# Performance work log

Measured on AMD Instinct MI355X. Metric: run time of the kernel, lower is better.

Reference implementation:

```python
import jax, jax.numpy as jnp
import numpy as np

B, S, E, H = 4, 2048, 512, 8
DH = E // H
EPS = 1e-5

def _ln(x, g, b):
    m = jnp.mean(x, axis=-1, keepdims=True)
    v = jnp.var(x, axis=-1, keepdims=True)
    return (x - m) * jax.lax.rsqrt(v + EPS) * g + b

def setup_inputs() -> dict:
    key = jax.random.key(0)
    ks = jax.random.split(key, 8)
    sc = 0.02
    return {
        "x": jax.random.normal(ks[0], (B, S, E), dtype=jnp.float32),
        "ln1_g": jnp.ones((E,), jnp.float32),
        "ln1_b": jnp.zeros((E,), jnp.float32),
        "in_proj_w": sc * jax.random.normal(ks[1], (3 * E, E), jnp.float32),
        "in_proj_b": jnp.zeros((3 * E,), jnp.float32),
        "out_w": sc * jax.random.normal(ks[2], (E, E), jnp.float32),
        "out_b": jnp.zeros((E,), jnp.float32),
        "ln2_g": jnp.ones((E,), jnp.float32),
        "ln2_b": jnp.zeros((E,), jnp.float32),
        "fc1_w": sc * jax.random.normal(ks[3], (E, E), jnp.float32),
        "fc1_b": jnp.zeros((E,), jnp.float32),
        "fc2_w": sc * jax.random.normal(ks[4], (E, E), jnp.float32),
        "fc2_b": jnp.zeros((E,), jnp.float32),
    }

def reference(x, ln1_g, ln1_b, in_proj_w, in_proj_b, out_w, out_b,
              ln2_g, ln2_b, fc1_w, fc1_b, fc2_w, fc2_b):
    # pre-LN
    z = _ln(x, ln1_g, ln1_b)
    # qkv projection (torch MHA packed in_proj: [3E, E])
    qkv = z @ in_proj_w.T + in_proj_b          # [B,S,3E]
    q, k, v = jnp.split(qkv, 3, axis=-1)
    q = q.reshape(B, S, H, DH)
    k = k.reshape(B, S, H, DH)
    v = v.reshape(B, S, H, DH)
    scores = jnp.einsum("bqhd,bkhd->bhqk", q, k) / np.sqrt(DH).astype(np.float32)
    causal = jnp.triu(jnp.ones((S, S), dtype=bool), k=1)  # True = masked
    neg = jnp.finfo(scores.dtype).min
    scores = jnp.where(causal, neg, scores)
    attn = jax.nn.softmax(scores, axis=-1)      # [B,H,S,S]
    ctx = jnp.einsum("bhqk,bkhd->bqhd", attn, v).reshape(B, S, E)
    attn_out = ctx @ out_w.T + out_b
    # torch MHA with need_weights=True averages over heads by default
    attn_weights = jnp.mean(attn, axis=1)       # [B,S,S]
    z2 = x + attn_out
    y = _ln(z2, ln2_g, ln2_b)
    y = jax.nn.leaky_relu(y @ fc1_w.T + fc1_b, negative_slope=0.01)
    y = y @ fc2_w.T + fc2_b
    y = y + z2
    return (y, attn_weights)
```

## Files before the change

### kernel.cpp

```cpp
#include <hip/hip_runtime.h>

typedef short bf16x8 __attribute__((ext_vector_type(8)));
typedef float f32x4 __attribute__((ext_vector_type(4)));
typedef unsigned short u16x8 __attribute__((ext_vector_type(8)));

#define NB 4
#define SQ 2048
#define EM 512
#define NH 8
#define DHD 64
#define QSCALE 0.1803368801111731f

__device__ __forceinline__ unsigned short f2bf(float x) {
  unsigned u = __float_as_uint(x);
  u += 0x7FFFu + ((u >> 16) & 1u);
  return (unsigned short)(u >> 16);
}

__device__ __forceinline__ int sw8(int row, int col8) { return col8 ^ ((row & 7) << 3); }

__device__ __forceinline__ void glds16(const void* g, void* l) {
  __builtin_amdgcn_global_load_lds(
      (const __attribute__((address_space(1))) void*)g,
      (__attribute__((address_space(3))) void*)l, 16, 0, 0);
}

__global__ __launch_bounds__(256) void f2bf4_kernel(
    const float* __restrict__ w0, const float* __restrict__ w1,
    const float* __restrict__ w2, const float* __restrict__ w3,
    unsigned short* __restrict__ o0, unsigned short* __restrict__ o1,
    unsigned short* __restrict__ o2, unsigned short* __restrict__ o3) {
  int i = (blockIdx.x * 256 + threadIdx.x) * 8;
  const float* src;
  unsigned short* dst;
  int off;
  if (i < 786432) { src = w0; dst = o0; off = i; }
  else if (i < 1048576) { src = w1; dst = o1; off = i - 786432; }
  else if (i < 1310720) { src = w2; dst = o2; off = i - 1048576; }
  else { src = w3; dst = o3; off = i - 1310720; }
  f32x4 a = *(const f32x4*)(src + off);
  f32x4 b = *(const f32x4*)(src + off + 4);
  u16x8 o;
#pragma unroll
  for (int j = 0; j < 4; ++j) { o[j] = f2bf(a[j]); o[j + 4] = f2bf(b[j]); }
  *(u16x8*)(dst + off) = o;
}

__global__ __launch_bounds__(256) void ln_kernel(const float* __restrict__ x,
                                                 const float* __restrict__ g,
                                                 const float* __restrict__ bb,
                                                 unsigned short* __restrict__ out) {
  int tid = threadIdx.x;
  int row = blockIdx.x * 4 + (tid >> 6);
  int lane = tid & 63;
  size_t base = (size_t)row * EM + lane * 8;
  f32x4 v0 = *(const f32x4*)(x + base);
  f32x4 v1 = *(const f32x4*)(x + base + 4);
  float s = 0.f, q = 0.f;
#pragma unroll
  for (int j = 0; j < 4; ++j) { s += v0[j] + v1[j]; q += v0[j] * v0[j] + v1[j] * v1[j]; }
#pragma unroll
  for (int m = 1; m < 64; m <<= 1) { s += __shfl_xor(s, m); q += __shfl_xor(q, m); }
  float mean = s * (1.f / EM);
  float var = q * (1.f / EM) - mean * mean;
  float rs = rsqrtf(var + 1e-5f);
  f32x4 g0 = *(const f32x4*)(g + lane * 8), g1 = *(const f32x4*)(g + lane * 8 + 4);
  f32x4 b0 = *(const f32x4*)(bb + lane * 8), b1 = *(const f32x4*)(bb + lane * 8 + 4);
  u16x8 o;
#pragma unroll
  for (int j = 0; j < 4; ++j) {
    o[j] = f2bf((v0[j] - mean) * rs * g0[j] + b0[j]);
    o[j + 4] = f2bf((v1[j] - mean) * rs * g1[j] + b1[j]);
  }
  *(u16x8*)(out + base) = o;
}

template <bool LEAKY, bool RESID, bool OUTF32, bool QKV>
__global__ __launch_bounds__(256) void gemm64(
    const unsigned short* __restrict__ A, const unsigned short* __restrict__ Bm,
    const float* __restrict__ bias, const float* __restrict__ resid,
    float* __restrict__ outf, unsigned short* __restrict__ outh,
    unsigned short* __restrict__ qo, unsigned short* __restrict__ ko,
    unsigned short* __restrict__ vo, int M, int N, int K) {
  __shared__ unsigned short As[2][64][64];
  __shared__ unsigned short Bs[2][64][64];
  int m0 = blockIdx.x * 64, n0 = blockIdx.y * 64;
  int t = threadIdx.x;
  int wv = t >> 6, ln = t & 63, lg = ln >> 4, lr = ln & 15;
  int rsub = ln >> 3;
  int csw = ((ln & 7) ^ rsub) * 8;
  f32x4 acc[4];
#pragma unroll
  for (int c = 0; c < 4; ++c)
#pragma unroll
    for (int r = 0; r < 4; ++r) acc[c][r] = 0.f;

  const unsigned short* ag0 = A + (size_t)(m0 + wv * 16 + rsub) * K + csw;
  const unsigned short* ag1 = A + (size_t)(m0 + wv * 16 + 8 + rsub) * K + csw;
  const unsigned short* bg0 = Bm + (size_t)(n0 + wv * 16 + rsub) * K + csw;
  const unsigned short* bg1 = Bm + (size_t)(n0 + wv * 16 + 8 + rsub) * K + csw;

  glds16(ag0, &As[0][wv * 16][0]);
  glds16(ag1, &As[0][wv * 16 + 8][0]);
  glds16(bg0, &Bs[0][wv * 16][0]);
  glds16(bg1, &Bs[0][wv * 16 + 8][0]);

  int nk = K >> 6;
  for (int ki = 0; ki < nk; ++ki) {
    int cur = ki & 1;
    __syncthreads();
    if (ki + 1 < nk) {
      int nb = cur ^ 1;
      int ko_ = (ki + 1) * 64;
      glds16(ag0 + ko_, &As[nb][wv * 16][0]);
      glds16(ag1 + ko_, &As[nb][wv * 16 + 8][0]);
      glds16(bg0 + ko_, &Bs[nb][wv * 16][0]);
      glds16(bg1 + ko_, &Bs[nb][wv * 16 + 8][0]);
    }
#pragma unroll
    for (int kk = 0; kk < 64; kk += 32) {
      int arw = wv * 16 + lr;
      bf16x8 af = *(const bf16x8*)&As[cur][arw][sw8(arw, kk + lg * 8)];
#pragma unroll
      for (int c = 0; c < 4; ++c) {
        int brw = c * 16 + lr;
        bf16x8 bf = *(const bf16x8*)&Bs[cur][brw][sw8(brw, kk + lg * 8)];
        acc[c] = __builtin_amdgcn_mfma_f32_16x16x32_bf16(af, bf, acc[c], 0, 0, 0);
      }
    }
  }
#pragma unroll
  for (int c = 0; c < 4; ++c) {
    int C_ = n0 + c * 16 + lr;
    float bv = bias[C_];
#pragma unroll
    for (int r = 0; r < 4; ++r) {
      int R_ = m0 + wv * 16 + lg * 4 + r;
      float v = acc[c][r] + bv;
      if (LEAKY) v = v > 0.f ? v : 0.01f * v;
      if (RESID) v += resid[(size_t)R_ * N + C_];
      if (QKV) {
        int which = C_ >> 9, f = C_ & 511, h = f >> 6, d = f & 63;
        int b_ = R_ >> 11, s_ = R_ & 2047;
        if (which == 0) {
          qo[(((size_t)b_ * NH + h) * SQ + s_) * DHD + d] = f2bf(v * QSCALE);
        } else if (which == 1) {
          ko[(((size_t)b_ * NH + h) * SQ + s_) * DHD + d] = f2bf(v);
        } else {
          vo[(((size_t)b_ * NH + h) * DHD + d) * SQ + s_] = f2bf(v);
        }
      } else if (OUTF32) {
        outf[(size_t)R_ * N + C_] = v;
      } else {
        outh[(size_t)R_ * N + C_] = f2bf(v);
      }
    }
  }
}

__global__ __launch_bounds__(256) void gemm128qkv(
    const unsigned short* __restrict__ A, const unsigned short* __restrict__ Bm,
    const float* __restrict__ bias, unsigned short* __restrict__ qo,
    unsigned short* __restrict__ ko, unsigned short* __restrict__ vo, int K) {
  __shared__ unsigned short As[2][128][32];
  __shared__ unsigned short Bs[2][128][32];
  int lin = blockIdx.x;
  int xcd = lin & 7, idx = lin >> 3;
  int m0 = (xcd * 8 + (idx & 7)) * 128;
  int n0 = (idx >> 3) * 128;
  int t = threadIdx.x;
  int wv = t >> 6, ln = t & 63, lg = ln >> 4, lr = ln & 15;
  int wr = wv >> 1, wc = wv & 1;
  int row16 = ln >> 2, chunk = (ln & 3) * 8;
  f32x4 acc[4][4];
#pragma unroll
  for (int m = 0; m < 4; ++m)
#pragma unroll
    for (int n = 0; n < 4; ++n)
#pragma unroll
      for (int r = 0; r < 4; ++r) acc[m][n][r] = 0.f;

  const unsigned short* agA = A + (size_t)(m0 + wv * 16 + row16) * K + chunk;
  const unsigned short* agB = A + (size_t)(m0 + 64 + wv * 16 + row16) * K + chunk;
  const unsigned short* bgA = Bm + (size_t)(n0 + wv * 16 + row16) * K + chunk;
  const unsigned short* bgB = Bm + (size_t)(n0 + 64 + wv * 16 + row16) * K + chunk;

  glds16(agA, &As[0][wv * 16][0]);
  glds16(agB, &As[0][64 + wv * 16][0]);
  glds16(bgA, &Bs[0][wv * 16][0]);
  glds16(bgB, &Bs[0][64 + wv * 16][0]);

  int nk = K >> 5;
  for (int ki = 0; ki < nk; ++ki) {
    int cur = ki & 1;
    __syncthreads();
    if (ki + 1 < nk) {
      int nb = cur ^ 1;
      int ko_ = (ki + 1) * 32;
      glds16(agA + ko_, &As[nb][wv * 16][0]);
      glds16(agB + ko_, &As[nb][64 + wv * 16][0]);
      glds16(bgA + ko_, &Bs[nb][wv * 16][0]);
      glds16(bgB + ko_, &Bs[nb][64 + wv * 16][0]);
    }
    bf16x8 af[4], bfr[4];
#pragma unroll
    for (int m = 0; m < 4; ++m)
      af[m] = *(const bf16x8*)&As[cur][wr * 64 + m * 16 + lr][lg * 8];
#pragma unroll
    for (int n = 0; n < 4; ++n)
      bfr[n] = *(const bf16x8*)&Bs[cur][wc * 64 + n * 16 + lr][lg * 8];
#pragma unroll
    for (int m = 0; m < 4; ++m)
#pragma unroll
      for (int n = 0; n < 4; ++n)
        acc[m][n] = __builtin_amdgcn_mfma_f32_16x16x32_bf16(af[m], bfr[n], acc[m][n], 0, 0, 0);
  }

#pragma unroll
  for (int n = 0; n < 4; ++n) {
    int C_ = n0 + wc * 64 + n * 16 + lr;
    float bv = bias[C_];
#pragma unroll
    for (int m = 0; m < 4; ++m) {
#pragma unroll
      for (int r = 0; r < 4; ++r) {
        int R_ = m0 + wr * 64 + m * 16 + lg * 4 + r;
        float v = acc[m][n][r] + bv;
        int which = C_ >> 9, f = C_ & 511, h = f >> 6, d = f & 63;
        int b_ = R_ >> 11, s_ = R_ & 2047;
        if (which == 0) {
          qo[(((size_t)b_ * NH + h) * SQ + s_) * DHD + d] = f2bf(v * QSCALE);
        } else if (which == 1) {
          ko[(((size_t)b_ * NH + h) * SQ + s_) * DHD + d] = f2bf(v);
        } else {
          vo[(((size_t)b_ * NH + h) * DHD + d) * SQ + s_] = f2bf(v);
        }
      }
    }
  }
}

__global__ __launch_bounds__(256) void flash_kernel(
    const unsigned short* __restrict__ Q, const unsigned short* __restrict__ Kb,
    const unsigned short* __restrict__ Vt, unsigned short* __restrict__ ctx,
    float* __restrict__ mstat, float* __restrict__ lstat) {
  __shared__ unsigned short Ks[2][64][64];
  __shared__ unsigned short Vs[2][64][64];
  __shared__ unsigned short Ps[4][16][64];
  int lin = blockIdx.x;
  int xcd = lin & 7, idx = lin >> 3;
  int qt = 31 - (idx >> 2);
  int grp = xcd + 8 * (idx & 3);
  int h = grp & 7, b = grp >> 3;
  int qb = qt * 64;
  int t = threadIdx.x, wv = t >> 6, ln = t & 63, lg = ln >> 4, lr = ln & 15;
  int rsub = ln >> 3;
  int csw = ((ln & 7) ^ rsub) * 8;
  size_t headoff = ((size_t)b * NH + h) * SQ;
  const unsigned short* kg0 = Kb + (headoff + wv * 16 + rsub) * DHD + csw;
  const unsigned short* kg1 = Kb + (headoff + wv * 16 + 8 + rsub) * DHD + csw;
  const unsigned short* vg0 = Vt + (((size_t)b * NH + h) * DHD + wv * 16 + rsub) * SQ + csw;
  const unsigned short* vg1 = Vt + (((size_t)b * NH + h) * DHD + wv * 16 + 8 + rsub) * SQ + csw;

  const unsigned short* qrow = Q + (headoff + qb + wv * 16 + lr) * DHD;
  bf16x8 aq0 = *(const bf16x8*)(qrow + lg * 8);
  bf16x8 aq1 = *(const bf16x8*)(qrow + 32 + lg * 8);

  bf16x8 vones;
#pragma unroll
  for (int j = 0; j < 8; ++j) vones[j] = (lr == 0) ? (short)0x3F80 : (short)0;

  f32x4 cacc[4], lacc;
#pragma unroll
  for (int nd = 0; nd < 4; ++nd)
#pragma unroll
    for (int r = 0; r < 4; ++r) cacc[nd][r] = 0.f;
#pragma unroll
  for (int r = 0; r < 4; ++r) lacc[r] = 0.f;
  float mrun[4];
#pragma unroll
  for (int r = 0; r < 4; ++r) mrun[r] = -__builtin_inff();

  int nkt = qt + 1;
  glds16(kg0, &Ks[0][wv * 16][0]);
  glds16(kg1, &Ks[0][wv * 16 + 8][0]);
  glds16(vg0, &Vs[0][wv * 16][0]);
  glds16(vg1, &Vs[0][wv * 16 + 8][0]);

  for (int kt = 0; kt < nkt; ++kt) {
    int cur = kt & 1;
    __syncthreads();
    if (kt + 1 < nkt) {
      int nb = cur ^ 1;
      size_t ko_ = (size_t)(kt + 1) * 64;
      glds16(kg0 + ko_ * DHD, &Ks[nb][wv * 16][0]);
      glds16(kg1 + ko_ * DHD, &Ks[nb][wv * 16 + 8][0]);
      glds16(vg0 + ko_, &Vs[nb][wv * 16][0]);
      glds16(vg1 + ko_, &Vs[nb][wv * 16 + 8][0]);
    }

    float sv[4][4];
    __builtin_amdgcn_s_setprio(1);
#pragma unroll
    for (int nt = 0; nt < 4; ++nt) {
      f32x4 sf;
#pragma unroll
      for (int r = 0; r < 4; ++r) sf[r] = 0.f;
      int brw = nt * 16 + lr;
      bf16x8 bk0 = *(const bf16x8*)&Ks[cur][brw][sw8(brw, lg * 8)];
      bf16x8 bk1 = *(const bf16x8*)&Ks[cur][brw][sw8(brw, 32 + lg * 8)];
      sf = __builtin_amdgcn_mfma_f32_16x16x32_bf16(aq0, bk0, sf, 0, 0, 0);
      sf = __builtin_amdgcn_mfma_f32_16x16x32_bf16(aq1, bk1, sf, 0, 0, 0);
#pragma unroll
      for (int r = 0; r < 4; ++r) sv[nt][r] = sf[r];
    }
    __builtin_amdgcn_s_setprio(0);
    if (kt == nkt - 1) {
      int kbase = kt * 64;
#pragma unroll
      for (int nt = 0; nt < 4; ++nt) {
        int kcol = kbase + nt * 16 + lr;
#pragma unroll
        for (int r = 0; r < 4; ++r) {
          int qr = qb + wv * 16 + lg * 4 + r;
          if (kcol > qr) sv[nt][r] = -__builtin_inff();
        }
      }
    }

    float lmax[4];
    bool need = false;
#pragma unroll
    for (int r = 0; r < 4; ++r) {
      lmax[r] = fmaxf(fmaxf(sv[0][r], sv[1][r]), fmaxf(sv[2][r], sv[3][r]));
      need |= (lmax[r] > mrun[r] + 8.f);
    }
    if (__any(need)) {
#pragma unroll
      for (int r = 0; r < 4; ++r) {
        float tm = lmax[r];
#pragma unroll
        for (int m = 1; m < 16; m <<= 1) tm = fmaxf(tm, __shfl_xor(tm, m));
        float mn = fmaxf(mrun[r], tm);
        float sc = exp2f(mrun[r] - mn);
        mrun[r] = mn;
        lacc[r] *= sc;
#pragma unroll
        for (int nd = 0; nd < 4; ++nd) cacc[nd][r] *= sc;
      }
    }
#pragma unroll
    for (int r = 0; r < 4; ++r) {
      int prow = lg * 4 + r;
#pragma unroll
      for (int nt = 0; nt < 4; ++nt) {
        float p = exp2f(sv[nt][r] - mrun[r]);
        Ps[wv][prow][sw8(prow, nt * 16 + lr)] =
            (unsigned short)(__float_as_uint(p) >> 16);
      }
    }

    bf16x8 pf0 = *(const bf16x8*)&Ps[wv][lr][sw8(lr, lg * 8)];
    bf16x8 pf1 = *(const bf16x8*)&Ps[wv][lr][sw8(lr, 32 + lg * 8)];
    __builtin_amdgcn_s_setprio(1);
    lacc = __builtin_amdgcn_mfma_f32_16x16x32_bf16(pf0, vones, lacc, 0, 0, 0);
    lacc = __builtin_amdgcn_mfma_f32_16x16x32_bf16(pf1, vones, lacc, 0, 0, 0);
#pragma unroll
    for (int nd = 0; nd < 4; ++nd) {
      int vrw = nd * 16 + lr;
      bf16x8 vf0 = *(const bf16x8*)&Vs[cur][vrw][sw8(vrw, lg * 8)];
      bf16x8 vf1 = *(const bf16x8*)&Vs[cur][vrw][sw8(vrw, 32 + lg * 8)];
      cacc[nd] = __builtin_amdgcn_mfma_f32_16x16x32_bf16(pf0, vf0, cacc[nd], 0, 0, 0);
      cacc[nd] = __builtin_amdgcn_mfma_f32_16x16x32_bf16(pf1, vf1, cacc[nd], 0, 0, 0);
    }
    __builtin_amdgcn_s_setprio(0);
  }

  float inv[4];
#pragma unroll
  for (int r = 0; r < 4; ++r) inv[r] = 1.f / __shfl(lacc[r], ln & 48);
#pragma unroll
  for (int nd = 0; nd < 4; ++nd)
#pragma unroll
    for (int r = 0; r < 4; ++r) {
      size_t dst = ((size_t)b * SQ + qb + wv * 16 + lg * 4 + r) * EM + h * DHD + nd * 16 + lr;
      ctx[dst] = f2bf(cacc[nd][r] * inv[r]);
    }
  if (lr == 0) {
#pragma unroll
    for (int r = 0; r < 4; ++r) {
      int row = qb + wv * 16 + lg * 4 + r;
      mstat[headoff + row] = mrun[r];
      lstat[headoff + row] = 0.125f * inv[r];
    }
  }
}

__global__ __launch_bounds__(256) void attnw_kernel(
    const unsigned short* __restrict__ Q, const unsigned short* __restrict__ Kb,
    const float* __restrict__ mstat, const float* __restrict__ lstat,
    float* __restrict__ aw) {
  int lin = blockIdx.x;
  int xcd = lin & 7, slot = lin >> 3;
  int combo = xcd + 8 * (slot >> 5);
  int qt = slot & 31;
  int kt2 = combo & 15, b = combo >> 4;
  int qb = qt * 64, kb = kt2 * 128;
  int t = threadIdx.x;
  float* tile = aw + ((size_t)b * SQ + qb) * SQ + kb;
  if (2 * kt2 > qt) {
    int row = t >> 2, cbase = (t & 3) * 32;
    f32x4 z;
#pragma unroll
    for (int j = 0; j < 4; ++j) z[j] = 0.f;
    float* p = tile + (size_t)row * SQ + cbase;
#pragma unroll
    for (int j = 0; j < 8; ++j) *(f32x4*)(p + j * 4) = z;
    return;
  }
  __shared__ unsigned short Ks[2][2][64][64];
  int wv = t >> 6, ln = t & 63, lg = ln >> 4, lr = ln & 15;
  int rsub = ln >> 3;
  int csw = ((ln & 7) ^ rsub) * 8;
  size_t khstride = (size_t)SQ * DHD;
  const unsigned short* kg00 = Kb + (((size_t)b * NH) * SQ + kb + wv * 16 + rsub) * DHD + csw;
  const unsigned short* kg01 = kg00 + (size_t)8 * DHD;
  const unsigned short* kg10 = kg00 + (size_t)64 * DHD;
  const unsigned short* kg11 = kg00 + (size_t)72 * DHD;
  const unsigned short* qg = Q + (((size_t)b * NH) * SQ + qb + wv * 16 + lr) * DHD + lg * 8;
  size_t mbase = (size_t)b * NH * SQ + qb + wv * 16 + lg * 4;

  glds16(kg00, &Ks[0][0][wv * 16][0]);
  glds16(kg01, &Ks[0][0][wv * 16 + 8][0]);
  glds16(kg10, &Ks[0][1][wv * 16][0]);
  glds16(kg11, &Ks[0][1][wv * 16 + 8][0]);

  bf16x8 aqc0 = *(const bf16x8*)qg;
  bf16x8 aqc1 = *(const bf16x8*)(qg + 32);
  bf16x8 aqn0 = *(const bf16x8*)(qg + khstride);
  bf16x8 aqn1 = *(const bf16x8*)(qg + khstride + 32);
  float mmc[4], lic[4], mmn[4], lin_[4];
#pragma unroll
  for (int r = 0; r < 4; ++r) {
    mmc[r] = mstat[mbase + r];
    lic[r] = lstat[mbase + r];
    mmn[r] = mstat[mbase + SQ + r];
    lin_[r] = lstat[mbase + SQ + r];
  }

  f32x4 facc[2][4];
#pragma unroll
  for (int j = 0; j < 2; ++j)
#pragma unroll
    for (int nt = 0; nt < 4; ++nt)
#pragma unroll
      for (int r = 0; r < 4; ++r) facc[j][nt][r] = 0.f;

  for (int h = 0; h < NH; ++h) {
    int cur = h & 1;
    __syncthreads();
    if (h + 1 < NH) {
      size_t ho = (size_t)(h + 1) * khstride;
      glds16(kg00 + ho, &Ks[cur ^ 1][0][wv * 16][0]);
      glds16(kg01 + ho, &Ks[cur ^ 1][0][wv * 16 + 8][0]);
      glds16(kg10 + ho, &Ks[cur ^ 1][1][wv * 16][0]);
      glds16(kg11 + ho, &Ks[cur ^ 1][1][wv * 16 + 8][0]);
    }

#pragma unroll
    for (int nt = 0; nt < 4; ++nt) {
      int brw = nt * 16 + lr;
      f32x4 sf0, sf1;
#pragma unroll
      for (int r = 0; r < 4; ++r) { sf0[r] = 0.f; sf1[r] = 0.f; }
      bf16x8 bk00 = *(const bf16x8*)&Ks[cur][0][brw][sw8(brw, lg * 8)];
      bf16x8 bk01 = *(const bf16x8*)&Ks[cur][0][brw][sw8(brw, 32 + lg * 8)];
      bf16x8 bk10 = *(const bf16x8*)&Ks[cur][1][brw][sw8(brw, lg * 8)];
      bf16x8 bk11 = *(const bf16x8*)&Ks[cur][1][brw][sw8(brw, 32 + lg * 8)];
      sf0 = __builtin_amdgcn_mfma_f32_16x16x32_bf16(aqc0, bk00, sf0, 0, 0, 0);
      sf1 = __builtin_amdgcn_mfma_f32_16x16x32_bf16(aqc0, bk10, sf1, 0, 0, 0);
      sf0 = __builtin_amdgcn_mfma_f32_16x16x32_bf16(aqc1, bk01, sf0, 0, 0, 0);
      sf1 = __builtin_amdgcn_mfma_f32_16x16x32_bf16(aqc1, bk11, sf1, 0, 0, 0);
#pragma unroll
      for (int r = 0; r < 4; ++r) {
        facc[0][nt][r] += exp2f(sf0[r] - mmc[r]) * lic[r];
        facc[1][nt][r] += exp2f(sf1[r] - mmc[r]) * lic[r];
      }
    }

    aqc0 = aqn0; aqc1 = aqn1;
#pragma unroll
    for (int r = 0; r < 4; ++r) { mmc[r] = mmn[r]; lic[r] = lin_[r]; }
    if (h + 2 < NH) {
      aqn0 = *(const bf16x8*)(qg + (size_t)(h + 2) * khstride);
      aqn1 = *(const bf16x8*)(qg + (size_t)(h + 2) * khstride + 32);
#pragma unroll
      for (int r = 0; r < 4; ++r) {
        mmn[r] = mstat[mbase + (size_t)(h + 2) * SQ + r];
        lin_[r] = lstat[mbase + (size_t)(h + 2) * SQ + r];
      }
    }
  }

#pragma unroll
  for (int j = 0; j < 2; ++j) {
    int ktj = 2 * kt2 + j;
    bool fullmask = (ktj > qt);
    bool dg = (ktj == qt);
#pragma unroll
    for (int nt = 0; nt < 4; ++nt) {
      int kc = kb + j * 64 + nt * 16 + lr;
#pragma unroll
      for (int r = 0; r < 4; ++r) {
        int qr = qb + wv * 16 + lg * 4 + r;
        float v = (fullmask || (dg && kc > qr)) ? 0.f : facc[j][nt][r];
        tile[(size_t)(wv * 16 + lg * 4 + r) * SQ + j * 64 + nt * 16 + lr] = v;
      }
    }
  }
}

extern "C" void kernel_launch(void* const* d_in, const int* in_sizes, int n_in,
                              void* d_out, int out_size, void* d_ws, size_t ws_size,
                              hipStream_t stream) {
  (void)in_sizes; (void)n_in; (void)out_size; (void)ws_size;
  const float* x = (const float*)d_in[0];
  const float* ln1g = (const float*)d_in[1];
  const float* ln1b = (const float*)d_in[2];
  const float* wqkv = (const float*)d_in[3];
  const float* bqkv = (const float*)d_in[4];
  const float* wout = (const float*)d_in[5];
  const float* bout = (const float*)d_in[6];
  const float* ln2g = (const float*)d_in[7];
  const float* ln2b = (const float*)d_in[8];
  const float* wfc1 = (const float*)d_in[9];
  const float* bfc1 = (const float*)d_in[10];
  const float* wfc2 = (const float*)d_in[11];
  const float* bfc2 = (const float*)d_in[12];

  char* ws = (char*)d_ws;
  unsigned short* zctx = (unsigned short*)(ws);
  unsigned short* qb_ = (unsigned short*)(ws + 8388608);
  unsigned short* kb_ = (unsigned short*)(ws + 16777216);
  unsigned short* vb_ = (unsigned short*)(ws + 25165824);
  float* z2 = (float*)(ws + 33554432);
  float* mstat = (float*)(ws + 50331648);
  float* lstat = (float*)(ws + 50593792);
  unsigned short* wqkv_h = (unsigned short*)(ws + 50855936);
  unsigned short* wout_h = (unsigned short*)(ws + 52428800);
  unsigned short* wfc1_h = (unsigned short*)(ws + 52953088);
  unsigned short* wfc2_h = (unsigned short*)(ws + 53477376);
  unsigned short* y1 = qb_;
  unsigned short* h1 = kb_;

  float* outy = (float*)d_out;
  float* outw = outy + (size_t)NB * SQ * EM;

  f2bf4_kernel<<<768, 256, 0, stream>>>(wqkv, wout, wfc1, wfc2,
                                        wqkv_h, wout_h, wfc1_h, wfc2_h);

  ln_kernel<<<2048, 256, 0, stream>>>(x, ln1g, ln1b, zctx);
  gemm128qkv<<<768, 256, 0, stream>>>(zctx, wqkv_h, bqkv, qb_, kb_, vb_, 512);
  flash_kernel<<<1024, 256, 0, stream>>>(qb_, kb_, vb_, zctx, mstat, lstat);
  attnw_kernel<<<2048, 256, 0, stream>>>(qb_, kb_, mstat, lstat, outw);
  gemm64<false, true, true, false><<<dim3(128, 8), 256, 0, stream>>>(
      zctx, wout_h, bout, x, z2, nullptr, nullptr, nullptr, nullptr, 8192, 512, 512);
  ln_kernel<<<2048, 256, 0, stream>>>(z2, ln2g, ln2b, y1);
  gemm64<true, false, false, false><<<dim3(128, 8), 256, 0, stream>>>(
      y1, wfc1_h, bfc1, nullptr, nullptr, h1, nullptr, nullptr, nullptr, 8192, 512, 512);
  gemm64<false, true, true, false><<<dim3(128, 8), 256, 0, stream>>>(
      h1, wfc2_h, bfc2, z2, outy, nullptr, nullptr, nullptr, nullptr, 8192, 512, 512);
}
```

Before: 170.4 us.

## Pair causal q-tiles in attn-weights kernel and retile GEMMs with XCD-aware mapping

The attention-weights kernel now has each block handle two query tiles (qp and qp+16) against one key tile. This balances causal work across blocks and reuses the staged K tiles for both, halving the grid to 1024 blocks. The dense GEMMs are rewritten to use a 32-wide K step with a new swizzle and a 1D grid that keeps neighbouring M tiles on the same XCD. The risks are more registers for the doubled accumulators in the attention kernel and more barriers per GEMM from the smaller K step.

```diff
diff --git a/kernel.cpp b/kernel.cpp
--- a/kernel.cpp
+++ b/kernel.cpp
@@ -18,6 +18,7 @@
 }
 
 __device__ __forceinline__ int sw8(int row, int col8) { return col8 ^ ((row & 7) << 3); }
+__device__ __forceinline__ int sw32(int row, int lg) { return (lg ^ ((row >> 1) & 3)) * 8; }
 
 __device__ __forceinline__ void glds16(const void* g, void* l) {
   __builtin_amdgcn_global_load_lds(
@@ -75,58 +76,50 @@
   *(u16x8*)(out + base) = o;
 }
 
-template <bool LEAKY, bool RESID, bool OUTF32, bool QKV>
-__global__ __launch_bounds__(256) void gemm64(
+template <bool LEAKY, bool RESID, bool OUTF32>
+__global__ __launch_bounds__(256) void gemm64b(
     const unsigned short* __restrict__ A, const unsigned short* __restrict__ Bm,
     const float* __restrict__ bias, const float* __restrict__ resid,
-    float* __restrict__ outf, unsigned short* __restrict__ outh,
-    unsigned short* __restrict__ qo, unsigned short* __restrict__ ko,
-    unsigned short* __restrict__ vo, int M, int N, int K) {
-  __shared__ unsigned short As[2][64][64];
-  __shared__ unsigned short Bs[2][64][64];
-  int m0 = blockIdx.x * 64, n0 = blockIdx.y * 64;
+    float* __restrict__ outf, unsigned short* __restrict__ outh, int N, int K) {
+  __shared__ unsigned short As[2][64][32];
+  __shared__ unsigned short Bs[2][64][32];
+  int lin = blockIdx.x;
+  int xcd = lin & 7, idx = lin >> 3;
+  int m0 = (xcd * 16 + (idx & 15)) * 64;
+  int n0 = (idx >> 4) * 64;
   int t = threadIdx.x;
   int wv = t >> 6, ln = t & 63, lg = ln >> 4, lr = ln & 15;
-  int rsub = ln >> 3;
-  int csw = ((ln & 7) ^ rsub) * 8;
+  int row16 = ln >> 2;
+  int chs = ((ln & 3) ^ ((row16 >> 1) & 3)) * 8;
   f32x4 acc[4];
 #pragma unroll
   for (int c = 0; c < 4; ++c)
 #pragma unroll
     for (int r = 0; r < 4; ++r) acc[c][r] = 0.f;
 
-  const unsigned short* ag0 = A + (size_t)(m0 + wv * 16 + rsub) * K + csw;
-  const unsigned short* ag1 = A + (size_t)(m0 + wv * 16 + 8 + rsub) * K + csw;
-  const unsigned short* bg0 = Bm + (size_t)(n0 + wv * 16 + rsub) * K + csw;
-  const unsigned short* bg1 = Bm + (size_t)(n0 + wv * 16 + 8 + rsub) * K + csw;
-
-  glds16(ag0, &As[0][wv * 16][0]);
-  glds16(ag1, &As[0][wv * 16 + 8][0]);
-  glds16(bg0, &Bs[0][wv * 16][0]);
-  glds16(bg1, &Bs[0][wv * 16 + 8][0]);
-
-  int nk = K >> 6;
+  const unsigned short* ag = A + (size_t)(m0 + wv * 16 + row16) * K + chs;
+  const unsigned short* bg = Bm + (size_t)(n0 + wv * 16 + row16) * K + chs;
+
+  glds16(ag, &As[0][wv * 16][0]);
+  glds16(bg, &Bs[0][wv * 16][0]);
+
+  int nk = K >> 5;
   for (int ki = 0; ki < nk; ++ki) {
     int cur = ki & 1;
     __syncthreads();
     if (ki + 1 < nk) {
       int nb = cur ^ 1;
-      int ko_ = (ki + 1) * 64;
-      glds16(ag0 + ko_, &As[nb][wv * 16][0]);
-      glds16(ag1 + ko_, &As[nb][wv * 16 + 8][0]);
-      glds16(bg0 + ko_, &Bs[nb][wv * 16][0]);
-      glds16(bg1 + ko_, &Bs[nb][wv * 16 + 8][0]);
-    }
-#pragma unroll
-    for (int kk = 0; kk < 64; kk += 32) {
-      int arw = wv * 16 + lr;
-      bf16x8 af = *(const bf16x8*)&As[cur][arw][sw8(arw, kk + lg * 8)];
-#pragma unroll
-      for (int c = 0; c < 4; ++c) {
-        int brw = c * 16 + lr;
-        bf16x8 bf = *(const bf16x8*)&Bs[cur][brw][sw8(brw, kk + lg * 8)];
-        acc[c] = __builtin_amdgcn_mfma_f32_16x16x32_bf16(af, bf, acc[c], 0, 0, 0);
-      }
+      int ko_ = (ki + 1) * 32;
+      glds16(ag + ko_, &As[nb][wv * 16][0]);
+      glds16(bg + ko_, &Bs[nb][wv * 16][0]);
+    }
+    int arw = wv * 16 + lr;
+    bf16x8 af = *(const bf16x8*)&As[cur][arw][sw32(arw, lg)];
+#pragma unroll
+    for (int c = 0; c < 4; ++c) {
+      int brw = c * 16 + lr;
+      bf16x8 bf = *(const bf16x8*)&Bs[cur][brw][sw32(brw, lg)];
+      acc[c] = __builtin_amdgcn_mfma_f32_16x16x32_bf16(af, bf, acc[c], 0, 0, 0);
     }
   }
 #pragma unroll
@@ -139,17 +132,7 @@
       float v = acc[c][r] + bv;
       if (LEAKY) v = v > 0.f ? v : 0.01f * v;
       if (RESID) v += resid[(size_t)R_ * N + C_];
-      if (QKV) {
-        int which = C_ >> 9, f = C_ & 511, h = f >> 6, d = f & 63;
-        int b_ = R_ >> 11, s_ = R_ & 2047;
-        if (which == 0) {
-          qo[(((size_t)b_ * NH + h) * SQ + s_) * DHD + d] = f2bf(v * QSCALE);
-        } else if (which == 1) {
-          ko[(((size_t)b_ * NH + h) * SQ + s_) * DHD + d] = f2bf(v);
-        } else {
-          vo[(((size_t)b_ * NH + h) * DHD + d) * SQ + s_] = f2bf(v);
-        }
-      } else if (OUTF32) {
+      if (OUTF32) {
         outf[(size_t)R_ * N + C_] = v;
       } else {
         outh[(size_t)R_ * N + C_] = f2bf(v);
@@ -402,65 +385,65 @@
     float* __restrict__ aw) {
   int lin = blockIdx.x;
   int xcd = lin & 7, slot = lin >> 3;
-  int combo = xcd + 8 * (slot >> 5);
-  int qt = slot & 31;
+  int combo = xcd + 8 * (slot >> 4);
+  int qp = slot & 15;
   int kt2 = combo & 15, b = combo >> 4;
-  int qb = qt * 64, kb = kt2 * 128;
+  int kb = kt2 * 128;
   int t = threadIdx.x;
-  float* tile = aw + ((size_t)b * SQ + qb) * SQ + kb;
-  if (2 * kt2 > qt) {
+  int wv = t >> 6, ln = t & 63, lg = ln >> 4, lr = ln & 15;
+  int qb0 = qp * 64, qb1 = (qp + 16) * 64;
+  bool a0 = (2 * kt2 <= qp);
+  bool a1 = (2 * kt2 <= qp + 16);
+  {
     int row = t >> 2, cbase = (t & 3) * 32;
     f32x4 z;
 #pragma unroll
     for (int j = 0; j < 4; ++j) z[j] = 0.f;
-    float* p = tile + (size_t)row * SQ + cbase;
-#pragma unroll
-    for (int j = 0; j < 8; ++j) *(f32x4*)(p + j * 4) = z;
-    return;
+    if (!a0) {
+      float* p = aw + ((size_t)b * SQ + qb0 + row) * SQ + kb + cbase;
+#pragma unroll
+      for (int j = 0; j < 8; ++j) *(f32x4*)(p + j * 4) = z;
+    }
+    if (!a1) {
+      float* p = aw + ((size_t)b * SQ + qb1 + row) * SQ + kb + cbase;
+#pragma unroll
+      for (int j = 0; j < 8; ++j) *(f32x4*)(p + j * 4) = z;
+      return;
+    }
   }
   __shared__ unsigned short Ks[2][2][64][64];
-  int wv = t >> 6, ln = t & 63, lg = ln >> 4, lr = ln & 15;
   int rsub = ln >> 3;
   int csw = ((ln & 7) ^ rsub) * 8;
-  size_t khstride = (size_t)SQ * DHD;
+  size_t khs = (size_t)SQ * DHD;
   const unsigned short* kg00 = Kb + (((size_t)b * NH) * SQ + kb + wv * 16 + rsub) * DHD + csw;
   const unsigned short* kg01 = kg00 + (size_t)8 * DHD;
   const unsigned short* kg10 = kg00 + (size_t)64 * DHD;
   const unsigned short* kg11 = kg00 + (size_t)72 * DHD;
-  const unsigned short* qg = Q + (((size_t)b * NH) * SQ + qb + wv * 16 + lr) * DHD + lg * 8;
-  size_t mbase = (size_t)b * NH * SQ + qb + wv * 16 + lg * 4;
+  const unsigned short* qg0 = Q + (((size_t)b * NH) * SQ + qb0 + wv * 16 + lr) * DHD + lg * 8;
+  const unsigned short* qg1 = Q + (((size_t)b * NH) * SQ + qb1 + wv * 16 + lr) * DHD + lg * 8;
+  size_t mb0 = (size_t)b * NH * SQ + qb0 + wv * 16 + lg * 4;
+  size_t mb1 = (size_t)b * NH * SQ + qb1 + wv * 16 + lg * 4;
 
   glds16(kg00, &Ks[0][0][wv * 16][0]);
   glds16(kg01, &Ks[0][0][wv * 16 + 8][0]);
   glds16(kg10, &Ks[0][1][wv * 16][0]);
   glds16(kg11, &Ks[0][1][wv * 16 + 8][0]);
 
-  bf16x8 aqc0 = *(const bf16x8*)qg;
-  bf16x8 aqc1 = *(const bf16x8*)(qg + 32);
-  bf16x8 aqn0 = *(const bf16x8*)(qg + khstride);
-  bf16x8 aqn1 = *(const bf16x8*)(qg + khstride + 32);
-  float mmc[4], lic[4], mmn[4], lin_[4];
-#pragma unroll
-  for (int r = 0; r < 4; ++r) {
-    mmc[r] = mstat[mbase + r];
-    lic[r] = lstat[mbase + r];
-    mmn[r] = mstat[mbase + SQ + r];
-    lin_[r] = lstat[mbase + SQ + r];
-  }
-
-  f32x4 facc[2][4];
-#pragma unroll
-  for (int j = 0; j < 2; ++j)
-#pragma unroll
-    for (int nt = 0; nt < 4; ++nt)
-#pragma unroll
-      for (int r = 0; r < 4; ++r) facc[j][nt][r] = 0.f;
+  f32x4 facc[2][2][4];
+#pragma unroll
+  for (int qi = 0; qi < 2; ++qi)
+#pragma unroll
+    for (int j = 0; j < 2; ++j)
+#pragma unroll
+      for (int nt = 0; nt < 4; ++nt)
+#pragma unroll
+        for (int r = 0; r < 4; ++r) facc[qi][j][nt][r] = 0.f;
 
   for (int h = 0; h < NH; ++h) {
     int cur = h & 1;
     __syncthreads();
     if (h + 1 < NH) {
-      size_t ho = (size_t)(h + 1) * khstride;
+      size_t ho = (size_t)(h + 1) * khs;
       glds16(kg00 + ho, &Ks[cur ^ 1][0][wv * 16][0]);
       glds16(kg01 + ho, &Ks[cur ^ 1][0][wv * 16 + 8][0]);
       glds16(kg10 + ho, &Ks[cur ^ 1][1][wv * 16][0]);
@@ -468,53 +451,57 @@
     }
 
 #pragma unroll
-    for (int nt = 0; nt < 4; ++nt) {
-      int brw = nt * 16 + lr;
-      f32x4 sf0, sf1;
-#pragma unroll
-      for (int r = 0; r < 4; ++r) { sf0[r] = 0.f; sf1[r] = 0.f; }
-      bf16x8 bk00 = *(const bf16x8*)&Ks[cur][0][brw][sw8(brw, lg * 8)];
-      bf16x8 bk01 = *(const bf16x8*)&Ks[cur][0][brw][sw8(brw, 32 + lg * 8)];
-      bf16x8 bk10 = *(const bf16x8*)&Ks[cur][1][brw][sw8(brw, lg * 8)];
-      bf16x8 bk11 = *(const bf16x8*)&Ks[cur][1][brw][sw8(brw, 32 + lg * 8)];
-      sf0 = __builtin_amdgcn_mfma_f32_16x16x32_bf16(aqc0, bk00, sf0, 0, 0, 0);
-      sf1 = __builtin_amdgcn_mfma_f32_16x16x32_bf16(aqc0, bk10, sf1, 0, 0, 0);
-      sf0 = __builtin_amdgcn_mfma_f32_16x16x32_bf16(aqc1, bk01, sf0, 0, 0, 0);
-      sf1 = __builtin_amdgcn_mfma_f32_16x16x32_bf16(aqc1, bk11, sf1, 0, 0, 0);
-#pragma unroll
-      for (int r = 0; r < 4; ++r) {
-        facc[0][nt][r] += exp2f(sf0[r] - mmc[r]) * lic[r];
-        facc[1][nt][r] += exp2f(sf1[r] - mmc[r]) * lic[r];
-      }
-    }
-
-    aqc0 = aqn0; aqc1 = aqn1;
-#pragma unroll
-    for (int r = 0; r < 4; ++r) { mmc[r] = mmn[r]; lic[r] = lin_[r]; }
-    if (h + 2 < NH) {
-      aqn0 = *(const bf16x8*)(qg + (size_t)(h + 2) * khstride);
-      aqn1 = *(const bf16x8*)(qg + (size_t)(h + 2) * khstride + 32);
-#pragma unroll
-      for (int r = 0; r < 4; ++r) {
-        mmn[r] = mstat[mbase + (size_t)(h + 2) * SQ + r];
-        lin_[r] = lstat[mbase + (size_t)(h + 2) * SQ + r];
-      }
-    }
-  }
-
-#pragma unroll
-  for (int j = 0; j < 2; ++j) {
-    int ktj = 2 * kt2 + j;
-    bool fullmask = (ktj > qt);
-    bool dg = (ktj == qt);
-#pragma unroll
-    for (int nt = 0; nt < 4; ++nt) {
-      int kc = kb + j * 64 + nt * 16 + lr;
-#pragma unroll
-      for (int r = 0; r < 4; ++r) {
-        int qr = qb + wv * 16 + lg * 4 + r;
-        float v = (fullmask || (dg && kc > qr)) ? 0.f : facc[j][nt][r];
-        tile[(size_t)(wv * 16 + lg * 4 + r) * SQ + j * 64 + nt * 16 + lr] = v;
+    for (int qi = 0; qi < 2; ++qi) {
+      if (qi == 0 && !a0) continue;
+      const unsigned short* qg = qi ? qg1 : qg0;
+      size_t mb = qi ? mb1 : mb0;
+      bf16x8 qa = *(const bf16x8*)(qg + (size_t)h * khs);
+      bf16x8 qc = *(const bf16x8*)(qg + (size_t)h * khs + 32);
+      f32x4 mm = *(const f32x4*)&mstat[mb + (size_t)h * SQ];
+      f32x4 ll = *(const f32x4*)&lstat[mb + (size_t)h * SQ];
+#pragma unroll
+      for (int nt = 0; nt < 4; ++nt) {
+        int brw = nt * 16 + lr;
+        bf16x8 bk00 = *(const bf16x8*)&Ks[cur][0][brw][sw8(brw, lg * 8)];
+        bf16x8 bk01 = *(const bf16x8*)&Ks[cur][0][brw][sw8(brw, 32 + lg * 8)];
+        bf16x8 bk10 = *(const bf16x8*)&Ks[cur][1][brw][sw8(brw, lg * 8)];
+        bf16x8 bk11 = *(const bf16x8*)&Ks[cur][1][brw][sw8(brw, 32 + lg * 8)];
+        f32x4 s0, s1;
+#pragma unroll
+        for (int r = 0; r < 4; ++r) { s0[r] = 0.f; s1[r] = 0.f; }
+        s0 = __builtin_amdgcn_mfma_f32_16x16x32_bf16(qa, bk00, s0, 0, 0, 0);
+        s1 = __builtin_amdgcn_mfma_f32_16x16x32_bf16(qa, bk10, s1, 0, 0, 0);
+        s0 = __builtin_amdgcn_mfma_f32_16x16x32_bf16(qc, bk01, s0, 0, 0, 0);
+        s1 = __builtin_amdgcn_mfma_f32_16x16x32_bf16(qc, bk11, s1, 0, 0, 0);
+#pragma unroll
+        for (int r = 0; r < 4; ++r) {
+          facc[qi][0][nt][r] += exp2f(s0[r] - mm[r]) * ll[r];
+          facc[qi][1][nt][r] += exp2f(s1[r] - mm[r]) * ll[r];
+        }
+      }
+    }
+  }
+
+#pragma unroll
+  for (int qi = 0; qi < 2; ++qi) {
+    if (qi == 0 && !a0) continue;
+    int qt = qi ? (qp + 16) : qp;
+    int qbq = qt * 64;
+    float* tile = aw + ((size_t)b * SQ + qbq) * SQ + kb;
+#pragma unroll
+    for (int j = 0; j < 2; ++j) {
+      int ktj = 2 * kt2 + j;
+      bool fullmask = (ktj > qt);
+      bool dg = (ktj == qt);
+#pragma unroll
+      for (int nt = 0; nt < 4; ++nt) {
+        int kc = kb + j * 64 + nt * 16 + lr;
+#pragma unroll
+        for (int r = 0; r < 4; ++r) {
+          int qr = qbq + wv * 16 + lg * 4 + r;
+          float v = (fullmask || (dg && kc > qr)) ? 0.f : facc[qi][j][nt][r];
+          tile[(size_t)(wv * 16 + lg * 4 + r) * SQ + j * 64 + nt * 16 + lr] = v;
+        }
       }
     }
   }
@@ -562,12 +549,12 @@
   ln_kernel<<<2048, 256, 0, stream>>>(x, ln1g, ln1b, zctx);
   gemm128qkv<<<768, 256, 0, stream>>>(zctx, wqkv_h, bqkv, qb_, kb_, vb_, 512);
   flash_kernel<<<1024, 256, 0, stream>>>(qb_, kb_, vb_, zctx, mstat, lstat);
-  attnw_kernel<<<2048, 256, 0, stream>>>(qb_, kb_, mstat, lstat, outw);
-  gemm64<false, true, true, false><<<dim3(128, 8), 256, 0, stream>>>(
-      zctx, wout_h, bout, x, z2, nullptr, nullptr, nullptr, nullptr, 8192, 512, 512);
+  attnw_kernel<<<1024, 256, 0, stream>>>(qb_, kb_, mstat, lstat, outw);
+  gemm64b<false, true, true><<<1024, 256, 0, stream>>>(
+      zctx, wout_h, bout, x, z2, nullptr, 512, 512);
   ln_kernel<<<2048, 256, 0, stream>>>(z2, ln2g, ln2b, y1);
-  gemm64<true, false, false, false><<<dim3(128, 8), 256, 0, stream>>>(
-      y1, wfc1_h, bfc1, nullptr, nullptr, h1, nullptr, nullptr, nullptr, 8192, 512, 512);
-  gemm64<false, true, true, false><<<dim3(128, 8), 256, 0, stream>>>(
-      h1, wfc2_h, bfc2, z2, outy, nullptr, nullptr, nullptr, nullptr, 8192, 512, 512);
-}
+  gemm64b<true, false, false><<<1024, 256, 0, stream>>>(
+      y1, wfc1_h, bfc1, nullptr, nullptr, h1, 512, 512);
+  gemm64b<false, true, true><<<1024, 256, 0, stream>>>(
+      h1, wfc2_h, bfc2, z2, outy, nullptr, 512, 512);
+}
```

Result: slower. 182.6 us (+7.2%).
